# Kernel optimization log

Hardware: AMD Instinct MI355X
Metric: run time of the kernel (lower is better)

The kernel has to match this reference:

```python
import jax, jax.numpy as jnp
from jax import lax
import numpy as np

VOCAB = 100000
MAX_SEQ = 8192
DIM = 128
K = 5
STRIDE = 1
PAD = 2


def setup_inputs() -> dict:
    key = jax.random.key(0)
    ks = jax.random.split(key, 6)
    X = jax.random.randint(ks[0], (8, 8192), 0, VOCAB, dtype=jnp.int64)
    # nn.Linear(vocab, dim): weight (dim, vocab), bias (dim)
    W_lin = jax.random.normal(ks[1], (DIM, VOCAB), dtype=jnp.float32) * 0.02
    b_lin = jax.random.normal(ks[2], (DIM,), dtype=jnp.float32) * 0.02
    # nn.Conv1d(dim, dim, k): weight (out=dim, in=dim, k), bias (dim)
    W_conv = jax.random.normal(ks[3], (DIM, DIM, K), dtype=jnp.float32) * 0.02
    b_conv = jax.random.normal(ks[4], (DIM,), dtype=jnp.float32) * 0.02
    # nn.Embedding(max_seq_len, dim)
    pos_table = jax.random.normal(ks[5], (MAX_SEQ, DIM), dtype=jnp.float32) * 0.02
    return {"X": X, "W_lin": W_lin, "b_lin": b_lin,
            "W_conv": W_conv, "b_conv": b_conv, "pos_table": pos_table}


def reference(X, W_lin, b_lin, W_conv, b_conv, pos_table):
    # one_hot(X) @ W_lin.T + b_lin  ==  gather rows of W_lin.T
    emb = jnp.take(W_lin.T, X, axis=0) + b_lin          # (b, n, d)
    x = jnp.transpose(emb, (0, 2, 1))                   # (b, d, n)
    y = lax.conv_general_dilated(
        x, W_conv, window_strides=(STRIDE,), padding=[(PAD, PAD)],
        dimension_numbers=("NCH", "OIH", "NCH"))
    y = y + b_conv[None, :, None]                       # (b, d, n_out)
    tokens = jnp.transpose(y, (0, 2, 1))                # (b, n_out, d)
    n_out = tokens.shape[1]
    return tokens + pos_table[:n_out][None, :, :]
```

## Files before the change

kernel.cpp:

```cpp
#include <hip/hip_runtime.h>
#include <hip/hip_bf16.h>
#include <stdint.h>

#define VOCAB 100000
#define SEQ   8192
#define BATCH 8
#define DIM   128

#define WLT_BLOCKS 1563
#define WCONV_BLOCKS 320

typedef short bf16x8 __attribute__((ext_vector_type(8)));
typedef float f32x4  __attribute__((ext_vector_type(4)));

__device__ __forceinline__ ushort f2bf(float f) {
  union { float f; uint32_t u; } v; v.f = f;
  uint32_t u = v.u;
  return (ushort)((u + 0x7FFF + ((u >> 16) & 1)) >> 16);
}

__global__ __launch_bounds__(256) void prep(
    const float* __restrict__ wlin, const float* __restrict__ blin,
    const float* __restrict__ wconv, ushort* __restrict__ wlt,
    ushort* __restrict__ wcb) {
  __shared__ float tile[128 * 65];
  const int tid = threadIdx.x;

  if (blockIdx.x >= WLT_BLOCKS) {
    int e = (blockIdx.x - WLT_BLOCKS) * 256 + tid;
    int k = e / (DIM * DIM);
    int rem = e % (DIM * DIM);
    int d = rem / DIM, i = rem % DIM;
    wcb[e] = f2bf(wconv[(d * DIM + i) * 5 + k]);
    return;
  }

  const int t0 = blockIdx.x * 64;

  const int c4 = (tid & 15) * 4;
  const int rbase = tid >> 4;
  const bool cvalid = (t0 + c4) < VOCAB;
#pragma unroll
  for (int p = 0; p < 8; ++p) {
    int r = p * 16 + rbase;
    float4 v = make_float4(0.f, 0.f, 0.f, 0.f);
    if (cvalid) v = *(const float4*)(wlin + (size_t)r * VOCAB + t0 + c4);
    float* dst = &tile[r * 65 + c4];
    dst[0] = v.x; dst[1] = v.y; dst[2] = v.z; dst[3] = v.w;
  }
  __syncthreads();

  const int chunk = tid & 15;
  float bias8[8];
#pragma unroll
  for (int j = 0; j < 8; ++j) bias8[j] = blin[chunk * 8 + j];

#pragma unroll
  for (int p = 0; p < 4; ++p) {
    int tl = (tid >> 4) + p * 16;
    int t  = t0 + tl;
    if (t >= VOCAB) continue;
    ushort u[8];
#pragma unroll
    for (int j = 0; j < 8; ++j)
      u[j] = f2bf(tile[(chunk * 8 + j) * 65 + tl] + bias8[j]);
    *(uint4*)(wlt + (size_t)t * DIM + chunk * 8) = *(const uint4*)u;
  }
}

__global__ __launch_bounds__(256, 4) void conv_main(
    const int* __restrict__ X, const ushort* __restrict__ wlt,
    const ushort* __restrict__ wcb, const float* __restrict__ bconv,
    const float* __restrict__ pos, float* __restrict__ out) {
  __shared__ __align__(16) ushort Atile[68 * 136];

  const int tid   = threadIdx.x;
  const int bm    = blockIdx.x;
  const int batch = bm >> 7;
  const int nbase = (bm & 127) << 6;
  const int* Xb   = X + batch * SEQ;

  int  tok[5];
  bool valid[5];
#pragma unroll
  for (int it = 0; it < 5; ++it) {
    int c = tid + it * 256;
    int r = c >> 4;
    int n = nbase - 2 + r;
    bool v = (c < 1088) && (n >= 0) && (n < SEQ);
    valid[it] = v;
    tok[it] = v ? Xb[n] : 0;
  }
  uint4 val[5];
#pragma unroll
  for (int it = 0; it < 5; ++it) {
    int ch = (tid + it * 256) & 15;
    val[it] = valid[it] ? *(const uint4*)(wlt + (size_t)tok[it] * DIM + ch * 8)
                        : make_uint4(0u, 0u, 0u, 0u);
  }
#pragma unroll
  for (int it = 0; it < 5; ++it) {
    int c = tid + it * 256;
    if (c < 1088) {
      int r = c >> 4, ch = c & 15;
      *(uint4*)&Atile[r * 136 + ch * 8] = val[it];
    }
  }
  __syncthreads();

  const int wave = tid >> 6;
  const int lane = tid & 63;
  const int wm = (wave >> 1) << 5;
  const int wn = (wave & 1) << 6;
  const int lr = lane & 15;
  const int lq = lane >> 4;

  f32x4 acc[2][4];
#pragma unroll
  for (int a = 0; a < 2; ++a)
#pragma unroll
    for (int b = 0; b < 4; ++b) acc[a][b] = (f32x4)0.f;

#pragma unroll
  for (int k = 0; k < 5; ++k) {
#pragma unroll
    for (int kk = 0; kk < 4; ++kk) {
      bf16x8 B[4];
#pragma unroll
      for (int nt = 0; nt < 4; ++nt)
        B[nt] = *(const bf16x8*)(wcb +
            ((size_t)(k * DIM + wn + nt * 16 + lr) * DIM + kk * 32 + lq * 8));
      bf16x8 A[2];
#pragma unroll
      for (int mt = 0; mt < 2; ++mt)
        A[mt] = *(const bf16x8*)&Atile[(wm + mt * 16 + lr + k) * 136 + kk * 32 + lq * 8];
#pragma unroll
      for (int mt = 0; mt < 2; ++mt)
#pragma unroll
        for (int nt = 0; nt < 4; ++nt)
          acc[mt][nt] = __builtin_amdgcn_mfma_f32_16x16x32_bf16(
              A[mt], B[nt], acc[mt][nt], 0, 0, 0);
    }
  }

  float bc[4];
#pragma unroll
  for (int nt = 0; nt < 4; ++nt) bc[nt] = bconv[wn + nt * 16 + lr];
  float* outb = out + (size_t)batch * SEQ * DIM;
#pragma unroll
  for (int mt = 0; mt < 2; ++mt) {
#pragma unroll
    for (int rr = 0; rr < 4; ++rr) {
      int m = wm + mt * 16 + lq * 4 + rr;
      int gn = nbase + m;
      const float* posrow = pos + (size_t)gn * DIM;
      float* orow = outb + (size_t)gn * DIM;
#pragma unroll
      for (int nt = 0; nt < 4; ++nt) {
        int d = wn + nt * 16 + lr;
        orow[d] = acc[mt][nt][rr] + bc[nt] + posrow[d];
      }
    }
  }
}

extern "C" void kernel_launch(void* const* d_in, const int* in_sizes, int n_in,
                              void* d_out, int out_size, void* d_ws, size_t ws_size,
                              hipStream_t stream) {
  const int*   X     = (const int*)d_in[0];
  const float* wlin  = (const float*)d_in[1];
  const float* blin  = (const float*)d_in[2];
  const float* wconv = (const float*)d_in[3];
  const float* bconv = (const float*)d_in[4];
  const float* pos   = (const float*)d_in[5];
  float*       out   = (float*)d_out;

  ushort* wcb = (ushort*)d_ws;
  ushort* wlt = (ushort*)((char*)d_ws + 262144);

  hipLaunchKernelGGL(prep, dim3(WLT_BLOCKS + WCONV_BLOCKS), dim3(256), 0, stream,
                     wlin, blin, wconv, wlt, wcb);
  hipLaunchKernelGGL(conv_main, dim3(1024), dim3(256), 0, stream,
                     X, wlt, wcb, bconv, pos, out);
}
```

Measured before the change: 154.6 us.

## Gather embedding rows directly into MFMA registers per wave, drop shared tile

The conv kernel now gives each wave a 32-row by 128-column output tile. Embedding rows are gathered straight from global memory into MFMA A-operand registers for each of the 5 taps, so the shared-memory staging tile and the block barrier are gone. The goal is to remove LDS traffic and synchronisation and to double the output columns per wave so more work is done per B load. In exchange, each token row is re-fetched from global/L2 up to five times across taps, register pressure grows (the accumulator becomes 2x8), occupancy drops to 2 blocks per CU, and the grid is halved.

Measured after the change: 161.3 us. +4.3%, slower.

```diff
diff --git a/kernel.cpp b/kernel.cpp
--- a/kernel.cpp
+++ b/kernel.cpp
@@ -68,100 +68,95 @@
   }
 }
 
-__global__ __launch_bounds__(256, 4) void conv_main(
-    const int* __restrict__ X, const ushort* __restrict__ wlt,
+template <bool EDGE>
+__device__ __forceinline__ void conv_wave(
+    const int* __restrict__ Xb, const ushort* __restrict__ wlt,
     const ushort* __restrict__ wcb, const float* __restrict__ bconv,
-    const float* __restrict__ pos, float* __restrict__ out) {
-  __shared__ __align__(16) ushort Atile[68 * 136];
+    const float* __restrict__ pos, float* __restrict__ outb,
+    int n0, int lr, int lq) {
+  int  tok[2][5];
+  bool vld[2][5];
+#pragma unroll
+  for (int mt = 0; mt < 2; ++mt)
+#pragma unroll
+    for (int k = 0; k < 5; ++k) {
+      int n = n0 + mt * 16 + lr + k - 2;
+      bool v = EDGE ? (n >= 0 && n < SEQ) : true;
+      vld[mt][k] = v;
+      tok[mt][k] = v ? Xb[n] : 0;
+    }
 
-  const int tid   = threadIdx.x;
-  const int bm    = blockIdx.x;
-  const int batch = bm >> 7;
-  const int nbase = (bm & 127) << 6;
-  const int* Xb   = X + batch * SEQ;
+  f32x4 acc[2][8];
+#pragma unroll
+  for (int mt = 0; mt < 2; ++mt)
+#pragma unroll
+    for (int nt = 0; nt < 8; ++nt) acc[mt][nt] = (f32x4)0.f;
 
-  int  tok[5];
-  bool valid[5];
-#pragma unroll
-  for (int it = 0; it < 5; ++it) {
-    int c = tid + it * 256;
-    int r = c >> 4;
-    int n = nbase - 2 + r;
-    bool v = (c < 1088) && (n >= 0) && (n < SEQ);
-    valid[it] = v;
-    tok[it] = v ? Xb[n] : 0;
-  }
-  uint4 val[5];
-#pragma unroll
-  for (int it = 0; it < 5; ++it) {
-    int ch = (tid + it * 256) & 15;
-    val[it] = valid[it] ? *(const uint4*)(wlt + (size_t)tok[it] * DIM + ch * 8)
-                        : make_uint4(0u, 0u, 0u, 0u);
-  }
-#pragma unroll
-  for (int it = 0; it < 5; ++it) {
-    int c = tid + it * 256;
-    if (c < 1088) {
-      int r = c >> 4, ch = c & 15;
-      *(uint4*)&Atile[r * 136 + ch * 8] = val[it];
-    }
-  }
-  __syncthreads();
-
-  const int wave = tid >> 6;
-  const int lane = tid & 63;
-  const int wm = (wave >> 1) << 5;
-  const int wn = (wave & 1) << 6;
-  const int lr = lane & 15;
-  const int lq = lane >> 4;
-
-  f32x4 acc[2][4];
-#pragma unroll
-  for (int a = 0; a < 2; ++a)
-#pragma unroll
-    for (int b = 0; b < 4; ++b) acc[a][b] = (f32x4)0.f;
-
+  const int colA = lq * 8;
 #pragma unroll
   for (int k = 0; k < 5; ++k) {
+    bf16x8 A[2][4];
+#pragma unroll
+    for (int mt = 0; mt < 2; ++mt)
+#pragma unroll
+      for (int kk = 0; kk < 4; ++kk) {
+        bf16x8 v = *(const bf16x8*)(wlt + ((size_t)tok[mt][k] << 7) + kk * 32 + colA);
+        A[mt][kk] = (EDGE && !vld[mt][k]) ? (bf16x8)(short)0 : v;
+      }
 #pragma unroll
     for (int kk = 0; kk < 4; ++kk) {
-      bf16x8 B[4];
+      bf16x8 B[8];
 #pragma unroll
-      for (int nt = 0; nt < 4; ++nt)
+      for (int nt = 0; nt < 8; ++nt)
         B[nt] = *(const bf16x8*)(wcb +
-            ((size_t)(k * DIM + wn + nt * 16 + lr) * DIM + kk * 32 + lq * 8));
-      bf16x8 A[2];
-#pragma unroll
-      for (int mt = 0; mt < 2; ++mt)
-        A[mt] = *(const bf16x8*)&Atile[(wm + mt * 16 + lr + k) * 136 + kk * 32 + lq * 8];
+            ((size_t)(k * DIM + nt * 16 + lr) * DIM + kk * 32 + colA));
 #pragma unroll
       for (int mt = 0; mt < 2; ++mt)
 #pragma unroll
-        for (int nt = 0; nt < 4; ++nt)
+        for (int nt = 0; nt < 8; ++nt)
           acc[mt][nt] = __builtin_amdgcn_mfma_f32_16x16x32_bf16(
-              A[mt], B[nt], acc[mt][nt], 0, 0, 0);
+              A[mt][kk], B[nt], acc[mt][nt], 0, 0, 0);
     }
   }
 
-  float bc[4];
+  float bc[8];
 #pragma unroll
-  for (int nt = 0; nt < 4; ++nt) bc[nt] = bconv[wn + nt * 16 + lr];
-  float* outb = out + (size_t)batch * SEQ * DIM;
+  for (int nt = 0; nt < 8; ++nt) bc[nt] = bconv[nt * 16 + lr];
 #pragma unroll
   for (int mt = 0; mt < 2; ++mt) {
 #pragma unroll
     for (int rr = 0; rr < 4; ++rr) {
-      int m = wm + mt * 16 + lq * 4 + rr;
-      int gn = nbase + m;
+      int gn = n0 + mt * 16 + lq * 4 + rr;
       const float* posrow = pos + (size_t)gn * DIM;
       float* orow = outb + (size_t)gn * DIM;
 #pragma unroll
-      for (int nt = 0; nt < 4; ++nt) {
-        int d = wn + nt * 16 + lr;
+      for (int nt = 0; nt < 8; ++nt) {
+        int d = nt * 16 + lr;
         orow[d] = acc[mt][nt][rr] + bc[nt] + posrow[d];
       }
     }
   }
+}
+
+__global__ __launch_bounds__(256, 2) void conv_main(
+    const int* __restrict__ X, const ushort* __restrict__ wlt,
+    const ushort* __restrict__ wcb, const float* __restrict__ bconv,
+    const float* __restrict__ pos, float* __restrict__ out) {
+  const int tid  = threadIdx.x;
+  const int wave = tid >> 6;
+  const int lane = tid & 63;
+  const int lr   = lane & 15;
+  const int lq   = lane >> 4;
+  const int gw    = blockIdx.x * 4 + wave;
+  const int batch = gw >> 8;
+  const int n0    = (gw & 255) << 5;
+  const int* Xb   = X + batch * SEQ;
+  float* outb     = out + (size_t)batch * SEQ * DIM;
+
+  if (n0 == 0 || n0 == SEQ - 32)
+    conv_wave<true>(Xb, wlt, wcb, bconv, pos, outb, n0, lr, lq);
+  else
+    conv_wave<false>(Xb, wlt, wcb, bconv, pos, outb, n0, lr, lq);
 }
 
 extern "C" void kernel_launch(void* const* d_in, const int* in_sizes, int n_in,
@@ -180,6 +175,6 @@
 
   hipLaunchKernelGGL(prep, dim3(WLT_BLOCKS + WCONV_BLOCKS), dim3(256), 0, stream,
                      wlin, blin, wconv, wlt, wcb);
-  hipLaunchKernelGGL(conv_main, dim3(1024), dim3(256), 0, stream,
+  hipLaunchKernelGGL(conv_main, dim3(512), dim3(256), 0, stream,
                      X, wlt, wcb, bconv, pos, out);
 }
```
